# Performance work log

Hardware: AMD Instinct MI355X
Metric: run time of the kernel (lower is better)

Reference implementation:

```python
import jax, jax.numpy as jnp
import numpy as np

N_NODES = 40000
N_EDGES = 400000
N_GRAPHS = 64
CONV_DIM = 64
N_FEAT = 9
EDGE_DIM = 3
Z_DIM = 2 * CONV_DIM + EDGE_DIM  # 131


def setup_inputs() -> dict:
    key = jax.random.key(0)
    ks = jax.random.split(key, 32)
    def lin(k, fan_in, fan_out):
        b = 1.0 / np.sqrt(fan_in)
        kw, kb = jax.random.split(k)
        return (jax.random.uniform(kw, (fan_in, fan_out), jnp.float32, -b, b),
                jax.random.uniform(kb, (fan_out,), jnp.float32, -b, b))
    inp = {}
    inp['x'] = jax.random.normal(ks[0], (N_NODES, N_FEAT), jnp.float32)
    inp['edge_index_1'] = jax.random.randint(ks[1], (2, N_EDGES), 0, N_NODES, jnp.int32)
    inp['edge_index_2'] = jax.random.randint(ks[2], (2, N_EDGES), 0, N_NODES, jnp.int32)
    inp['weight_1'] = jax.random.normal(ks[3], (N_EDGES, EDGE_DIM), jnp.float32)
    inp['weight_2'] = jax.random.normal(ks[4], (N_EDGES, EDGE_DIM), jnp.float32)
    # sorted graph ids: 64 graphs of 625 nodes each
    inp['batch'] = jnp.repeat(jnp.arange(N_GRAPHS, dtype=jnp.int32), N_NODES // N_GRAPHS)
    # parameters (stored [in, out])
    inp['fc1_w'], inp['fc1_b'] = lin(ks[5], N_FEAT, CONV_DIM)
    inp['lin_f_w'], inp['lin_f_b'] = lin(ks[6], Z_DIM, CONV_DIM)
    inp['lin_s_w'], inp['lin_s_b'] = lin(ks[7], Z_DIM, CONV_DIM)
    inp['gru_w_ih'], inp['gru_b_ih'] = lin(ks[8], CONV_DIM, 3 * CONV_DIM)  # gate order r,z,n
    inp['gru_w_hh'], inp['gru_b_hh'] = lin(ks[9], CONV_DIM, 3 * CONV_DIM)
    inp['fcs_w'], inp['fcs_b'] = lin(ks[10], CONV_DIM, CONV_DIM)
    inp['fc2c_w'], inp['fc2c_b'] = lin(ks[11], CONV_DIM, 64)
    inp['fc3c_w'], inp['fc3c_b'] = lin(ks[12], 64, 2)
    inp['fc2d_w'], inp['fc2d_b'] = lin(ks[13], CONV_DIM, 64)
    inp['fc3d_w'], inp['fc3d_b'] = lin(ks[14], 64, 2)
    return inp


def _cgconv(x, edge_index, edge_attr, wf, bf, ws, bs):
    # CGConv, flow='target_to_source': x_i = x[row], x_j = x[col], aggregate (mean) at row
    row, col = edge_index[0], edge_index[1]
    z = jnp.concatenate([x[row], x[col], edge_attr], axis=-1)       # [E, 131]
    msg = jax.nn.sigmoid(z @ wf + bf) * jax.nn.softplus(z @ ws + bs)  # [E, C]
    agg = jax.ops.segment_sum(msg, row, num_segments=x.shape[0])
    cnt = jax.ops.segment_sum(jnp.ones((msg.shape[0],), msg.dtype), row, num_segments=x.shape[0])
    return x + agg / jnp.maximum(cnt, 1.0)[:, None]                  # residual


def _gru_step(xt, h, w_ih, w_hh, b_ih, b_hh):
    gi = xt @ w_ih + b_ih
    gh = h @ w_hh + b_hh
    ir, iz, inn = jnp.split(gi, 3, axis=-1)
    hr, hz, hn = jnp.split(gh, 3, axis=-1)
    r = jax.nn.sigmoid(ir + hr)
    zg = jax.nn.sigmoid(iz + hz)
    n = jnp.tanh(inn + r * hn)
    return (1.0 - zg) * n + zg * h


def reference(x, edge_index_1, edge_index_2, weight_1, weight_2, batch,
              fc1_w, fc1_b, lin_f_w, lin_f_b, lin_s_w, lin_s_b,
              gru_w_ih, gru_b_ih, gru_w_hh, gru_b_hh,
              fcs_w, fcs_b, fc2c_w, fc2c_b, fc3c_w, fc3c_b,
              fc2d_w, fc2d_b, fc3d_w, fc3d_b):
    x = jax.nn.relu(x @ fc1_w + fc1_b)          # dropout inactive (eval)
    h = x
    for _ in range(3):                          # 3 GRU refinement iterations
        m = jax.nn.relu(_cgconv(x, edge_index_2, weight_2, lin_f_w, lin_f_b, lin_s_w, lin_s_b))
        m = jax.nn.relu(_cgconv(m, edge_index_1, weight_1, lin_f_w, lin_f_b, lin_s_w, lin_s_b))
        h = _gru_step(m, h, gru_w_ih, gru_w_hh, gru_b_ih, gru_b_hh)
        x = h
    # first node index of each graph (batch is sorted)
    idx_ct = jnp.searchsorted(batch, jnp.arange(N_GRAPHS, dtype=batch.dtype))
    xg = x[idx_ct]                              # [B, C]
    xg = jax.nn.relu(xg @ fcs_w + fcs_b)
    xc = jax.nn.relu(xg @ fc2c_w + fc2c_b)
    x_class = jax.nn.sigmoid(xc @ fc3c_w + fc3c_b)
    xd = jax.nn.relu(xg @ fc2d_w + fc2d_b)
    x_delta = xd @ fc3d_w + fc3d_b
    return (x_class, x_delta)
```

## Files before the change

kernel.cpp:

```cpp
#include <hip/hip_runtime.h>
#include <hip/hip_bf16.h>
#include <hip/hip_fp16.h>
#include <math.h>

constexpr int NE = 400000;
constexpr int NN = 40000;
constexpr int CD = 64;
constexpr int NGRAPH = 64;
constexpr int SCAN_BLOCKS = (NN + 255) / 256;
constexpr int EBLK = (NE + 255) / 256;

typedef _Float16 f16x8 __attribute__((ext_vector_type(8)));
typedef float f32x4 __attribute__((ext_vector_type(4)));

__global__ void k_fc1(const float* __restrict__ x,
                      const float* __restrict__ w,
                      const float* __restrict__ b,
                      float* __restrict__ out) {
    int i = blockIdx.x * 256 + threadIdx.x;
    if (i >= NN * CD) return;
    int n = i >> 6, c = i & 63;
    float acc = b[c];
    #pragma unroll
    for (int k = 0; k < 9; ++k)
        acc = fmaf(x[n * 9 + k], w[k * 64 + c], acc);
    out[i] = fmaxf(acc, 0.f);
}

__global__ void k_count2(const int* __restrict__ ei1, const int* __restrict__ ei2,
                         int* __restrict__ cnt1, int* __restrict__ cnt2) {
    const int b = blockIdx.x;
    const bool s2 = (b >= EBLK);
    const int* ei = s2 ? ei2 : ei1;
    int* cnt = s2 ? cnt2 : cnt1;
    int e = (s2 ? b - EBLK : b) * 256 + threadIdx.x;
    if (e >= NE) return;
    atomicAdd(&cnt[ei[e]], 1);
}

__global__ void k_scan_part2(const int* __restrict__ cnt1, const int* __restrict__ cnt2,
                             int* __restrict__ part1, int* __restrict__ part2) {
    __shared__ int red[256];
    const int b = blockIdx.x;
    const bool s2 = (b >= SCAN_BLOCKS);
    const int* cnt = s2 ? cnt2 : cnt1;
    int* partials = s2 ? part2 : part1;
    const int bb = s2 ? b - SCAN_BLOCKS : b;
    const int tid = threadIdx.x;
    const int i = bb * 256 + tid;
    red[tid] = (i < NN) ? cnt[i] : 0;
    __syncthreads();
    for (int s = 128; s > 0; s >>= 1) {
        if (tid < s) red[tid] += red[tid + s];
        __syncthreads();
    }
    if (tid == 0) partials[bb] = red[0];
}

__global__ void k_scan_mid2(const int* __restrict__ part1, const int* __restrict__ part2,
                            int* __restrict__ offs1, int* __restrict__ offs2) {
    __shared__ int part[256];
    const bool s2 = (blockIdx.x == 1);
    const int* partials = s2 ? part2 : part1;
    int* offs = s2 ? offs2 : offs1;
    const int tid = threadIdx.x;
    const int v = (tid < SCAN_BLOCKS) ? partials[tid] : 0;
    part[tid] = v;
    __syncthreads();
    for (int off = 1; off < 256; off <<= 1) {
        int t = (tid >= off) ? part[tid - off] : 0;
        __syncthreads();
        part[tid] += t;
        __syncthreads();
    }
    if (tid < SCAN_BLOCKS) offs[tid] = part[tid] - v;
}

__global__ void k_scan_fill2(const int* __restrict__ cnt1, const int* __restrict__ cnt2,
                             const int* __restrict__ offs1, const int* __restrict__ offs2,
                             int* __restrict__ rs1, int* __restrict__ rs2,
                             int* __restrict__ cur1, int* __restrict__ cur2) {
    __shared__ int part[256];
    const int b = blockIdx.x;
    const bool s2 = (b >= SCAN_BLOCKS);
    const int* cnt = s2 ? cnt2 : cnt1;
    const int* offs = s2 ? offs2 : offs1;
    int* row_start = s2 ? rs2 : rs1;
    int* cursor = s2 ? cur2 : cur1;
    const int bb = s2 ? b - SCAN_BLOCKS : b;
    const int tid = threadIdx.x;
    const int i = bb * 256 + tid;
    const int v = (i < NN) ? cnt[i] : 0;
    part[tid] = v;
    __syncthreads();
    for (int off = 1; off < 256; off <<= 1) {
        int t = (tid >= off) ? part[tid - off] : 0;
        __syncthreads();
        part[tid] += t;
        __syncthreads();
    }
    const int excl = part[tid] - v + offs[bb];
    if (i < NN) { row_start[i] = excl; cursor[i] = excl; }
    if (i == NN - 1) row_start[NN] = NE;
}

__global__ void k_scatgath2(const int* __restrict__ ei1, const int* __restrict__ ei2,
                            const float* __restrict__ w1, const float* __restrict__ w2,
                            int* __restrict__ cur1, int* __restrict__ cur2,
                            uint4* __restrict__ rec1, uint4* __restrict__ rec2) {
    const int b = blockIdx.x;
    const bool s2 = (b >= EBLK);
    const int* ei = s2 ? ei2 : ei1;
    const float* ew = s2 ? w2 : w1;
    int* cursor = s2 ? cur2 : cur1;
    uint4* rec = s2 ? rec2 : rec1;
    int e = (s2 ? b - EBLK : b) * 256 + threadIdx.x;
    if (e >= NE) return;
    const int r = ei[e];
    const int c = ei[NE + e];
    const int pos = atomicAdd(&cursor[r], 1);
    const __half2 h01 = __floats2half2_rn(ew[3 * e], ew[3 * e + 1]);
    const __half2 h2  = __floats2half2_rn(ew[3 * e + 2], 0.f);
    rec[pos] = make_uint4((unsigned)(((r & 7) << 28) | c),
                          *(const unsigned*)&h01, *(const unsigned*)&h2, 0u);
}

__global__ void k_wt16(const float* __restrict__ lfw, const float* __restrict__ lsw,
                       _Float16* __restrict__ Wt) {
    const int k = blockIdx.x;
    const int c = threadIdx.x;
    float v;
    if (c < 64)       v = lfw[k * 64 + c];
    else if (c < 128) v = lsw[k * 64 + (c - 64)];
    else if (c < 192) v = lfw[(64 + k) * 64 + (c - 128)];
    else              v = lsw[(64 + k) * 64 + (c - 192)];
    Wt[c * 64 + k] = (_Float16)v;
}

__global__ void k_wtg16(const float* __restrict__ wih, const float* __restrict__ whh,
                        _Float16* __restrict__ WtG) {
    const int i = blockIdx.x * 256 + threadIdx.x;
    const int c = i >> 6, k = i & 63;
    const float v = (c < 192) ? wih[k * 192 + c] : whh[k * 192 + (c - 192)];
    WtG[c * 64 + k] = (_Float16)v;
}

__launch_bounds__(256, 4)
__global__ void k_proj_mfma(const float* __restrict__ x,
                            const _Float16* __restrict__ Wt,
                            const float* __restrict__ bfp, const float* __restrict__ bsp,
                            float* __restrict__ Pi, __half2* __restrict__ Pj16) {
    __shared__ _Float16 xs16[32][72];
    const int tid = threadIdx.x;
    const int n0 = blockIdx.x * 32;
    {
        const int n = tid >> 3, k0 = (tid & 7) * 8;
        const float4 a = *(const float4*)&x[(size_t)(n0 + n) * 64 + k0];
        const float4 b = *(const float4*)&x[(size_t)(n0 + n) * 64 + k0 + 4];
        f16x8 v;
        v[0] = (_Float16)a.x; v[1] = (_Float16)a.y; v[2] = (_Float16)a.z; v[3] = (_Float16)a.w;
        v[4] = (_Float16)b.x; v[5] = (_Float16)b.y; v[6] = (_Float16)b.z; v[7] = (_Float16)b.w;
        *(f16x8*)&xs16[n][k0] = v;
    }
    __syncthreads();
    const int l  = tid & 63;
    const int w  = tid >> 6;
    const int lr = l & 15;
    const int kb = l >> 4;
    const int nt = w & 1;
    const f16x8 A0 = *(const f16x8*)&xs16[nt * 16 + lr][kb * 8];
    const f16x8 A1 = *(const f16x8*)&xs16[nt * 16 + lr][32 + kb * 8];
    const int orow = n0 + nt * 16 + kb * 4;

    if (w < 2) {
        for (int ct = 0; ct < 8; ++ct) {
            const int col = ct * 16 + lr;
            const f16x8 B0 = *(const f16x8*)&Wt[col * 64 + kb * 8];
            const f16x8 B1 = *(const f16x8*)&Wt[col * 64 + 32 + kb * 8];
            f32x4 acc = {0.f, 0.f, 0.f, 0.f};
            acc = __builtin_amdgcn_mfma_f32_16x16x32_f16(A0, B0, acc, 0, 0, 0);
            acc = __builtin_amdgcn_mfma_f32_16x16x32_f16(A1, B1, acc, 0, 0, 0);
            const float bias = (col < 64) ? bfp[col] : bsp[col - 64];
            #pragma unroll
            for (int r = 0; r < 4; ++r)
                Pi[(size_t)(orow + r) * 128 + col] = acc[r] + bias;
        }
    } else {
        for (int pt = 0; pt < 4; ++pt) {
            const int colF = 128 + pt * 16 + lr;
            const int colS = 192 + pt * 16 + lr;
            const f16x8 BF0 = *(const f16x8*)&Wt[colF * 64 + kb * 8];
            const f16x8 BF1 = *(const f16x8*)&Wt[colF * 64 + 32 + kb * 8];
            const f16x8 BS0 = *(const f16x8*)&Wt[colS * 64 + kb * 8];
            const f16x8 BS1 = *(const f16x8*)&Wt[colS * 64 + 32 + kb * 8];
            f32x4 aF = {0.f, 0.f, 0.f, 0.f}, aS = {0.f, 0.f, 0.f, 0.f};
            aF = __builtin_amdgcn_mfma_f32_16x16x32_f16(A0, BF0, aF, 0, 0, 0);
            aF = __builtin_amdgcn_mfma_f32_16x16x32_f16(A1, BF1, aF, 0, 0, 0);
            aS = __builtin_amdgcn_mfma_f32_16x16x32_f16(A0, BS0, aS, 0, 0, 0);
            aS = __builtin_amdgcn_mfma_f32_16x16x32_f16(A1, BS1, aS, 0, 0, 0);
            const int cj = pt * 16 + lr;
            #pragma unroll
            for (int r = 0; r < 4; ++r)
                Pj16[(size_t)(orow + r) * 64 + cj] = __floats2half2_rn((float)aF[r], (float)aS[r]);
        }
    }
}

__launch_bounds__(256, 8)
__global__ void k_edge_range(const __half2* __restrict__ Pj,
                             const float* __restrict__ Pi,
                             const uint4* __restrict__ rec,
                             const float* __restrict__ wfe, const float* __restrict__ wse,
                             const int* __restrict__ rs,
                             const float* __restrict__ xin, float* __restrict__ out) {
    __shared__ __align__(8) __half2 piH[8][64];
    __shared__ __align__(16) float accS[8][8][64];
    __shared__ int rsS[9];
    const int tid = threadIdx.x;
    const int hw = tid >> 5;
    const int hb = hw & 1;
    const int wv = tid >> 6;
    const int c2 = (tid & 31) * 2;
    const int r0 = blockIdx.x * 8;
    for (int i = tid; i < 512; i += 256) {
        const int row = i >> 6, ch = i & 63;
        piH[row][ch] = __floats2half2_rn(Pi[(size_t)(r0 + row) * 128 + ch],
                                         Pi[(size_t)(r0 + row) * 128 + 64 + ch]);
    }
    for (int i = tid; i < 4096; i += 256)
        ((float*)accS)[i] = 0.f;
    if (tid < 9) rsS[tid] = rs[r0 + tid];
    __syncthreads();
    const float wf0a = wfe[c2],       wf0b = wfe[c2 + 1];
    const float wf1a = wfe[64 + c2],  wf1b = wfe[64 + c2 + 1];
    const float wf2a = wfe[128 + c2], wf2b = wfe[128 + c2 + 1];
    const float ws0a = wse[c2],       ws0b = wse[c2 + 1];
    const float ws1a = wse[64 + c2],  ws1b = wse[64 + c2 + 1];
    const float ws2a = wse[128 + c2], ws2b = wse[128 + c2 + 1];
    const int pbeg = rsS[0], pend = rsS[8];

#define EDGE_BODY(P)                                                              \
    {                                                                             \
        const uint4 rv = rec[P];                                                  \
        const float2 e01 = __half22float2(*(const __half2*)&rv.y);                \
        const float2 e2x = __half22float2(*(const __half2*)&rv.z);                \
        const int row = rv.x >> 28;                                               \
        const int joff = (int)((rv.x & 0x0FFFFFFFu) << 6) | c2;                   \
        const uint2 Jraw = *(const uint2*)(Pj + joff);                            \
        const float2 Ja = __half22float2(*(const __half2*)&Jraw.x);               \
        const float2 Jb = __half22float2(*(const __half2*)&Jraw.y);               \
        const uint2 PH = *(const uint2*)&piH[row][c2];                            \
        const float2 Pa = __half22float2(*(const __half2*)&PH.x);                 \
        const float2 Pb = __half22float2(*(const __half2*)&PH.y);                 \
        const float afa = Pa.x + Ja.x + e01.x * wf0a + e01.y * wf1a + e2x.x * wf2a; \
        const float asa = Pa.y + Ja.y + e01.x * ws0a + e01.y * ws1a + e2x.x * ws2a; \
        const float afb = Pb.x + Jb.x + e01.x * wf0b + e01.y * wf1b + e2x.x * wf2b; \
        const float asb = Pb.y + Jb.y + e01.x * ws0b + e01.y * ws1b + e2x.x * ws2b; \
        const float sga = __builtin_amdgcn_rcpf(1.f + __expf(-afa));              \
        const float spa = (asa > 20.f) ? asa : __logf(1.f + __expf(asa));         \
        const float sgb = __builtin_amdgcn_rcpf(1.f + __expf(-afb));              \
        const float spb = (asb > 20.f) ? asb : __logf(1.f + __expf(asb));         \
        float2 acc = *(const float2*)&accS[hw][row][c2];                          \
        acc.x = fmaf(sga, spa, acc.x);                                            \
        acc.y = fmaf(sgb, spb, acc.y);                                            \
        *(float2*)&accS[hw][row][c2] = acc;                                       \
    }

    int p0 = pbeg + 2 * wv;
    #pragma unroll 2
    for (; p0 + 2 <= pend; p0 += 8) {
        const int p = p0 + hb;
        EDGE_BODY(p)
    }
    {
        const int p = p0 + hb;
        if (p < pend) EDGE_BODY(p)
    }
#undef EDGE_BODY

    __syncthreads();
    for (int i = tid; i < 512; i += 256) {
        const int row = i >> 6, ch = i & 63;
        float s = 0.f;
        #pragma unroll
        for (int a = 0; a < 8; ++a) s += accS[a][row][ch];
        const int deg = rsS[row + 1] - rsS[row];
        const size_t o = (size_t)(r0 + row) * 64 + ch;
        out[o] = fmaxf(fmaf(s, 1.f / (float)max(deg, 1), xin[o]), 0.f);
    }
}

__global__ void k_gru_mfma(const float* __restrict__ m, float* __restrict__ h,
                           const _Float16* __restrict__ WtG,
                           const float* __restrict__ bih, const float* __restrict__ bhh) {
    __shared__ _Float16 ms16[32][72];
    __shared__ _Float16 hs16[32][72];
    __shared__ __align__(16) float hs32[32][64];
    const int tid = threadIdx.x;
    const int n0 = blockIdx.x * 32;
    {
        const int n = tid >> 3, k0 = (tid & 7) * 8;
        const float4 ma = *(const float4*)&m[(size_t)(n0 + n) * 64 + k0];
        const float4 mb = *(const float4*)&m[(size_t)(n0 + n) * 64 + k0 + 4];
        const float4 ha = *(const float4*)&h[(size_t)(n0 + n) * 64 + k0];
        const float4 hb = *(const float4*)&h[(size_t)(n0 + n) * 64 + k0 + 4];
        f16x8 mv, hv;
        mv[0] = (_Float16)ma.x; mv[1] = (_Float16)ma.y; mv[2] = (_Float16)ma.z; mv[3] = (_Float16)ma.w;
        mv[4] = (_Float16)mb.x; mv[5] = (_Float16)mb.y; mv[6] = (_Float16)mb.z; mv[7] = (_Float16)mb.w;
        hv[0] = (_Float16)ha.x; hv[1] = (_Float16)ha.y; hv[2] = (_Float16)ha.z; hv[3] = (_Float16)ha.w;
        hv[4] = (_Float16)hb.x; hv[5] = (_Float16)hb.y; hv[6] = (_Float16)hb.z; hv[7] = (_Float16)hb.w;
        *(f16x8*)&ms16[n][k0] = mv;
        *(f16x8*)&hs16[n][k0] = hv;
        *(float4*)&hs32[n][k0] = ha;
        *(float4*)&hs32[n][k0 + 4] = hb;
    }
    __syncthreads();
    const int l  = tid & 63;
    const int w  = tid >> 6;
    const int lr = l & 15;
    const int kb = l >> 4;
    const int nt = w & 1;
    const int cg = w >> 1;
    const f16x8 A0 = *(const f16x8*)&ms16[nt * 16 + lr][kb * 8];
    const f16x8 A1 = *(const f16x8*)&ms16[nt * 16 + lr][32 + kb * 8];
    const f16x8 H0 = *(const f16x8*)&hs16[nt * 16 + lr][kb * 8];
    const f16x8 H1 = *(const f16x8*)&hs16[nt * 16 + lr][32 + kb * 8];
    const int orow = n0 + nt * 16 + kb * 4;
    const int lrow = nt * 16 + kb * 4;

    #pragma unroll
    for (int t = 0; t < 2; ++t) {
        const int ct = cg + t * 2;
        const int c = ct * 16 + lr;
        const f16x8 BiR0 = *(const f16x8*)&WtG[(c)       * 64 + kb * 8];
        const f16x8 BiR1 = *(const f16x8*)&WtG[(c)       * 64 + 32 + kb * 8];
        const f16x8 BiZ0 = *(const f16x8*)&WtG[(64 + c)  * 64 + kb * 8];
        const f16x8 BiZ1 = *(const f16x8*)&WtG[(64 + c)  * 64 + 32 + kb * 8];
        const f16x8 BiN0 = *(const f16x8*)&WtG[(128 + c) * 64 + kb * 8];
        const f16x8 BiN1 = *(const f16x8*)&WtG[(128 + c) * 64 + 32 + kb * 8];
        const f16x8 BhR0 = *(const f16x8*)&WtG[(192 + c) * 64 + kb * 8];
        const f16x8 BhR1 = *(const f16x8*)&WtG[(192 + c) * 64 + 32 + kb * 8];
        const f16x8 BhZ0 = *(const f16x8*)&WtG[(256 + c) * 64 + kb * 8];
        const f16x8 BhZ1 = *(const f16x8*)&WtG[(256 + c) * 64 + 32 + kb * 8];
        const f16x8 BhN0 = *(const f16x8*)&WtG[(320 + c) * 64 + kb * 8];
        const f16x8 BhN1 = *(const f16x8*)&WtG[(320 + c) * 64 + 32 + kb * 8];
        f32x4 aIR = {0,0,0,0}, aIZ = {0,0,0,0}, aIN = {0,0,0,0};
        f32x4 aHR = {0,0,0,0}, aHZ = {0,0,0,0}, aHN = {0,0,0,0};
        aIR = __builtin_amdgcn_mfma_f32_16x16x32_f16(A0, BiR0, aIR, 0, 0, 0);
        aIR = __builtin_amdgcn_mfma_f32_16x16x32_f16(A1, BiR1, aIR, 0, 0, 0);
        aIZ = __builtin_amdgcn_mfma_f32_16x16x32_f16(A0, BiZ0, aIZ, 0, 0, 0);
        aIZ = __builtin_amdgcn_mfma_f32_16x16x32_f16(A1, BiZ1, aIZ, 0, 0, 0);
        aIN = __builtin_amdgcn_mfma_f32_16x16x32_f16(A0, BiN0, aIN, 0, 0, 0);
        aIN = __builtin_amdgcn_mfma_f32_16x16x32_f16(A1, BiN1, aIN, 0, 0, 0);
        aHR = __builtin_amdgcn_mfma_f32_16x16x32_f16(H0, BhR0, aHR, 0, 0, 0);
        aHR = __builtin_amdgcn_mfma_f32_16x16x32_f16(H1, BhR1, aHR, 0, 0, 0);
        aHZ = __builtin_amdgcn_mfma_f32_16x16x32_f16(H0, BhZ0, aHZ, 0, 0, 0);
        aHZ = __builtin_amdgcn_mfma_f32_16x16x32_f16(H1, BhZ1, aHZ, 0, 0, 0);
        aHN = __builtin_amdgcn_mfma_f32_16x16x32_f16(H0, BhN0, aHN, 0, 0, 0);
        aHN = __builtin_amdgcn_mfma_f32_16x16x32_f16(H1, BhN1, aHN, 0, 0, 0);
        const float bir = bih[c], biz = bih[64 + c], bin = bih[128 + c];
        const float bhr = bhh[c], bhz = bhh[64 + c], bhn = bhh[128 + c];
        #pragma unroll
        for (int r = 0; r < 4; ++r) {
            const float rg = 1.f / (1.f + __expf(-(((float)aIR[r] + bir) + ((float)aHR[r] + bhr))));
            const float zg = 1.f / (1.f + __expf(-(((float)aIZ[r] + biz) + ((float)aHZ[r] + bhz))));
            const float ng = tanhf(((float)aIN[r] + bin) + rg * ((float)aHN[r] + bhn));
            h[(size_t)(orow + r) * 64 + c] = (1.f - zg) * ng + zg * hs32[lrow + r][c];
        }
    }
}

__global__ void k_head(const float* __restrict__ h, const int* __restrict__ batch,
                       const float* __restrict__ fcsw, const float* __restrict__ fcsb,
                       const float* __restrict__ f2cw, const float* __restrict__ f2cb,
                       const float* __restrict__ f3cw, const float* __restrict__ f3cb,
                       const float* __restrict__ f2dw, const float* __restrict__ f2db,
                       const float* __restrict__ f3dw, const float* __restrict__ f3db,
                       float* __restrict__ out) {
    __shared__ float hsB[4096];
    __shared__ float waB[4096];
    __shared__ float wbB[4096];
    __shared__ float wcB[4096];
    __shared__ int sidx[64];
    const int tid = threadIdx.x;
    if (tid < 64) {
        int lo = 0, hi = NN;
        while (lo < hi) {
            int mid = (lo + hi) >> 1;
            if (batch[mid] < tid) lo = mid + 1; else hi = mid;
        }
        sidx[tid] = lo;
    }
    __syncthreads();
    for (int i = tid; i < 4096; i += 256) {
        int g = i >> 6, k = i & 63;
        hsB[i] = h[(size_t)sidx[g] * 64 + k];
        waB[i] = fcsw[i];
        wbB[i] = f2cw[i];
        wcB[i] = f2dw[i];
    }
    __syncthreads();
    float v[16];
    #pragma unroll
    for (int j = 0; j < 16; ++j) {
        const int i = j * 256 + tid, g = i >> 6, c = i & 63;
        float a = fcsb[c];
        for (int k = 0; k < 64; ++k) a = fmaf(hsB[g * 64 + k], waB[k * 64 + c], a);
        v[j] = fmaxf(a, 0.f);
    }
    __syncthreads();
    #pragma unroll
    for (int j = 0; j < 16; ++j) hsB[j * 256 + tid] = v[j];
    __syncthreads();
    float vc[16], vd[16];
    #pragma unroll
    for (int j = 0; j < 16; ++j) {
        const int i = j * 256 + tid, g = i >> 6, c = i & 63;
        float a1 = f2cb[c], a2 = f2db[c];
        for (int k = 0; k < 64; ++k) {
            const float xv = hsB[g * 64 + k];
            a1 = fmaf(xv, wbB[k * 64 + c], a1);
            a2 = fmaf(xv, wcB[k * 64 + c], a2);
        }
        vc[j] = fmaxf(a1, 0.f);
        vd[j] = fmaxf(a2, 0.f);
    }
    __syncthreads();
    #pragma unroll
    for (int j = 0; j < 16; ++j) {
        waB[j * 256 + tid] = vc[j];
        wbB[j * 256 + tid] = vd[j];
    }
    if (tid < 128) wcB[tid] = f3cw[tid];
    else           wcB[tid] = f3dw[tid - 128];
    __syncthreads();
    if (tid < 128) {
        int g = tid >> 1, j = tid & 1;
        float a = f3cb[j];
        for (int k = 0; k < 64; ++k) a = fmaf(waB[g * 64 + k], wcB[k * 2 + j], a);
        out[g * 2 + j] = 1.f / (1.f + expf(-a));
    } else {
        int t = tid - 128, g = t >> 1, j = t & 1;
        float a = f3db[j];
        for (int k = 0; k < 64; ++k) a = fmaf(wbB[g * 64 + k], wcB[128 + k * 2 + j], a);
        out[128 + g * 2 + j] = a;
    }
}

extern "C" void kernel_launch(void* const* d_in, const int* in_sizes, int n_in,
                              void* d_out, int out_size, void* d_ws, size_t ws_size,
                              hipStream_t stream) {
    (void)in_sizes; (void)n_in; (void)out_size; (void)ws_size;
    const float* x    = (const float*)d_in[0];
    const int* ei1    = (const int*)d_in[1];
    const int* ei2    = (const int*)d_in[2];
    const float* w1   = (const float*)d_in[3];
    const float* w2   = (const float*)d_in[4];
    const int* batch  = (const int*)d_in[5];
    const float* fc1w = (const float*)d_in[6];
    const float* fc1b = (const float*)d_in[7];
    const float* lfw  = (const float*)d_in[8];
    const float* lfb  = (const float*)d_in[9];
    const float* lsw  = (const float*)d_in[10];
    const float* lsb  = (const float*)d_in[11];
    const float* wih  = (const float*)d_in[12];
    const float* bih  = (const float*)d_in[13];
    const float* whh  = (const float*)d_in[14];
    const float* bhh  = (const float*)d_in[15];
    const float* fcsw = (const float*)d_in[16];
    const float* fcsb = (const float*)d_in[17];
    const float* f2cw = (const float*)d_in[18];
    const float* f2cb = (const float*)d_in[19];
    const float* f3cw = (const float*)d_in[20];
    const float* f3cb = (const float*)d_in[21];
    const float* f2dw = (const float*)d_in[22];
    const float* f2db = (const float*)d_in[23];
    const float* f3dw = (const float*)d_in[24];
    const float* f3db = (const float*)d_in[25];

    char* ws = (char*)d_ws;
    size_t off = 0;
    auto alloc = [&](size_t bytes) { char* p = ws + off; off += (bytes + 255) & ~size_t(255); return p; };
    float*   Pi    = (float*)alloc(size_t(NN) * 128 * 4);
    __half2* Pj16  = (__half2*)alloc(size_t(NN) * 64 * 4);
    float*   hbuf  = (float*)alloc(size_t(NN) * CD * 4);
    float*   mbuf  = (float*)alloc(size_t(NN) * CD * 4);
    _Float16* W16  = (_Float16*)alloc(256 * 64 * 2);
    _Float16* WG16 = (_Float16*)alloc(384 * 64 * 2);
    int*   cnt1  = (int*)alloc(size_t(NN) * 4);
    int*   cnt2  = (int*)alloc(size_t(NN) * 4);
    int*   rs1   = (int*)alloc(size_t(NN + 1) * 4);
    int*   rs2   = (int*)alloc(size_t(NN + 1) * 4);
    int*   cur1  = (int*)alloc(size_t(NN + 1) * 4);
    int*   cur2  = (int*)alloc(size_t(NN + 1) * 4);
    uint4* rec1  = (uint4*)alloc(size_t(NE) * 16);
    uint4* rec2  = (uint4*)alloc(size_t(NE) * 16);
    int*   part1 = (int*)alloc(256 * 4);
    int*   part2 = (int*)alloc(256 * 4);
    int*   offs1 = (int*)alloc(256 * 4);
    int*   offs2 = (int*)alloc(256 * 4);

    const int NB_NC = (NN * CD + 255) / 256;
    const int EDGE_BLOCKS = NN / 8;
    const int PROJ_BLOCKS = NN / 32;
    const int GRU_BLOCKS  = NN / 32;

    const float* lfe = lfw + 128 * 64;
    const float* lse = lsw + 128 * 64;

    hipMemsetAsync(cnt1, 0, size_t(NN) * 4 * 2 + 256, stream);
    k_count2<<<2 * EBLK, 256, 0, stream>>>(ei1, ei2, cnt1, cnt2);
    k_scan_part2<<<2 * SCAN_BLOCKS, 256, 0, stream>>>(cnt1, cnt2, part1, part2);
    k_scan_mid2<<<2, 256, 0, stream>>>(part1, part2, offs1, offs2);
    k_scan_fill2<<<2 * SCAN_BLOCKS, 256, 0, stream>>>(cnt1, cnt2, offs1, offs2, rs1, rs2, cur1, cur2);
    k_scatgath2<<<2 * EBLK, 256, 0, stream>>>(ei1, ei2, w1, w2, cur1, cur2, rec1, rec2);
    k_wt16<<<64, 256, 0, stream>>>(lfw, lsw, W16);
    k_wtg16<<<96, 256, 0, stream>>>(wih, whh, WG16);

    k_fc1<<<NB_NC, 256, 0, stream>>>(x, fc1w, fc1b, hbuf);

    for (int it = 0; it < 3; ++it) {
        k_proj_mfma<<<PROJ_BLOCKS, 256, 0, stream>>>(hbuf, W16, lfb, lsb, Pi, Pj16);
        k_edge_range<<<EDGE_BLOCKS, 256, 0, stream>>>(Pj16, Pi, rec2, lfe, lse, rs2, hbuf, mbuf);
        k_proj_mfma<<<PROJ_BLOCKS, 256, 0, stream>>>(mbuf, W16, lfb, lsb, Pi, Pj16);
        k_edge_range<<<EDGE_BLOCKS, 256, 0, stream>>>(Pj16, Pi, rec1, lfe, lse, rs1, mbuf, mbuf);
        k_gru_mfma<<<GRU_BLOCKS, 256, 0, stream>>>(mbuf, hbuf, WG16, bih, bhh);
    }

    k_head<<<1, 256, 0, stream>>>(hbuf, batch, fcsw, fcsb, f2cw, f2cb, f3cw, f3cb,
                                  f2dw, f2db, f3dw, f3db, (float*)d_out);
}
```

Measured before the change: 534.9 us.

## Replace per-row atomic scatter with two-level bucket sort for CSR edges

The edge scatter into CSR order now runs in two passes. The first pass scatters each edge into a 32-row bucket with a global atomic on a bucket cursor. The second pass sorts within each bucket using shared-memory atomics, replacing the per-row global atomics in the old scatter. This is meant to cut global atomic traffic and scattered 16-byte writes, at the cost of an extra temp buffer pass and two more kernel launches. It also raises the unroll factor of the edge aggregation loop from 2 to 4.

```diff
diff --git a/kernel.cpp b/kernel.cpp
--- a/kernel.cpp
+++ b/kernel.cpp
@@ -9,6 +9,7 @@
 constexpr int NGRAPH = 64;
 constexpr int SCAN_BLOCKS = (NN + 255) / 256;
 constexpr int EBLK = (NE + 255) / 256;
+constexpr int NBUCK = NN / 32;
 
 typedef _Float16 f16x8 __attribute__((ext_vector_type(8)));
 typedef float f32x4 __attribute__((ext_vector_type(4)));
@@ -78,15 +79,13 @@
 
 __global__ void k_scan_fill2(const int* __restrict__ cnt1, const int* __restrict__ cnt2,
                              const int* __restrict__ offs1, const int* __restrict__ offs2,
-                             int* __restrict__ rs1, int* __restrict__ rs2,
-                             int* __restrict__ cur1, int* __restrict__ cur2) {
+                             int* __restrict__ rs1, int* __restrict__ rs2) {
     __shared__ int part[256];
     const int b = blockIdx.x;
     const bool s2 = (b >= SCAN_BLOCKS);
     const int* cnt = s2 ? cnt2 : cnt1;
     const int* offs = s2 ? offs2 : offs1;
     int* row_start = s2 ? rs2 : rs1;
-    int* cursor = s2 ? cur2 : cur1;
     const int bb = s2 ? b - SCAN_BLOCKS : b;
     const int tid = threadIdx.x;
     const int i = bb * 256 + tid;
@@ -100,29 +99,60 @@
         __syncthreads();
     }
     const int excl = part[tid] - v + offs[bb];
-    if (i < NN) { row_start[i] = excl; cursor[i] = excl; }
+    if (i < NN) row_start[i] = excl;
     if (i == NN - 1) row_start[NN] = NE;
 }
 
-__global__ void k_scatgath2(const int* __restrict__ ei1, const int* __restrict__ ei2,
-                            const float* __restrict__ w1, const float* __restrict__ w2,
-                            int* __restrict__ cur1, int* __restrict__ cur2,
-                            uint4* __restrict__ rec1, uint4* __restrict__ rec2) {
+__global__ void k_bcur2(const int* __restrict__ rs1, const int* __restrict__ rs2,
+                        int* __restrict__ bcur1, int* __restrict__ bcur2) {
+    const int i = blockIdx.x * 256 + threadIdx.x;
+    if (i < NBUCK)      bcur1[i] = rs1[i * 32];
+    else if (i < 2 * NBUCK) bcur2[(i - NBUCK)] = rs2[(i - NBUCK) * 32];
+}
+
+__global__ void k_bucket2(const int* __restrict__ ei1, const int* __restrict__ ei2,
+                          const float* __restrict__ w1, const float* __restrict__ w2,
+                          int* __restrict__ bcur1, int* __restrict__ bcur2,
+                          uint4* __restrict__ tmp1, uint4* __restrict__ tmp2) {
     const int b = blockIdx.x;
     const bool s2 = (b >= EBLK);
     const int* ei = s2 ? ei2 : ei1;
     const float* ew = s2 ? w2 : w1;
-    int* cursor = s2 ? cur2 : cur1;
-    uint4* rec = s2 ? rec2 : rec1;
+    int* bcur = s2 ? bcur2 : bcur1;
+    uint4* tmp = s2 ? tmp2 : tmp1;
     int e = (s2 ? b - EBLK : b) * 256 + threadIdx.x;
     if (e >= NE) return;
     const int r = ei[e];
     const int c = ei[NE + e];
-    const int pos = atomicAdd(&cursor[r], 1);
+    const int pos = atomicAdd(&bcur[r >> 5], 1);
     const __half2 h01 = __floats2half2_rn(ew[3 * e], ew[3 * e + 1]);
     const __half2 h2  = __floats2half2_rn(ew[3 * e + 2], 0.f);
-    rec[pos] = make_uint4((unsigned)(((r & 7) << 28) | c),
+    tmp[pos] = make_uint4((unsigned)(((r & 31) << 26) | c),
                           *(const unsigned*)&h01, *(const unsigned*)&h2, 0u);
+}
+
+__global__ void k_bsort2(const uint4* __restrict__ tmp1, const uint4* __restrict__ tmp2,
+                         const int* __restrict__ rs1, const int* __restrict__ rs2,
+                         uint4* __restrict__ rec1, uint4* __restrict__ rec2) {
+    __shared__ int curs[32];
+    const int b = blockIdx.x;
+    const bool s2 = (b >= NBUCK);
+    const uint4* tmp = s2 ? tmp2 : tmp1;
+    const int* rs = s2 ? rs2 : rs1;
+    uint4* rec = s2 ? rec2 : rec1;
+    const int bb = s2 ? b - NBUCK : b;
+    const int R0 = bb * 32;
+    const int tid = threadIdx.x;
+    if (tid < 32) curs[tid] = rs[R0 + tid];
+    __syncthreads();
+    const int pbeg = rs[R0], pend = rs[R0 + 32];
+    for (int p = pbeg + tid; p < pend; p += 256) {
+        uint4 t = tmp[p];
+        const int lr = (int)(t.x >> 26);
+        const int pos = atomicAdd(&curs[lr], 1);
+        t.x = (unsigned)(((lr & 7) << 28) | (t.x & 0x03FFFFFFu));
+        rec[pos] = t;
+    }
 }
 
 __global__ void k_wt16(const float* __restrict__ lfw, const float* __restrict__ lsw,
@@ -267,7 +297,7 @@
     }
 
     int p0 = pbeg + 2 * wv;
-    #pragma unroll 2
+    #pragma unroll 4
     for (; p0 + 2 <= pend; p0 += 8) {
         const int p = p0 + hb;
         EDGE_BODY(p)
@@ -491,8 +521,10 @@
     int*   cnt2  = (int*)alloc(size_t(NN) * 4);
     int*   rs1   = (int*)alloc(size_t(NN + 1) * 4);
     int*   rs2   = (int*)alloc(size_t(NN + 1) * 4);
-    int*   cur1  = (int*)alloc(size_t(NN + 1) * 4);
-    int*   cur2  = (int*)alloc(size_t(NN + 1) * 4);
+    int*   bcur1 = (int*)alloc(size_t(NBUCK) * 4);
+    int*   bcur2 = (int*)alloc(size_t(NBUCK) * 4);
+    uint4* tmp1  = (uint4*)alloc(size_t(NE) * 16);
+    uint4* tmp2  = (uint4*)alloc(size_t(NE) * 16);
     uint4* rec1  = (uint4*)alloc(size_t(NE) * 16);
     uint4* rec2  = (uint4*)alloc(size_t(NE) * 16);
     int*   part1 = (int*)alloc(256 * 4);
@@ -512,8 +544,10 @@
     k_count2<<<2 * EBLK, 256, 0, stream>>>(ei1, ei2, cnt1, cnt2);
     k_scan_part2<<<2 * SCAN_BLOCKS, 256, 0, stream>>>(cnt1, cnt2, part1, part2);
     k_scan_mid2<<<2, 256, 0, stream>>>(part1, part2, offs1, offs2);
-    k_scan_fill2<<<2 * SCAN_BLOCKS, 256, 0, stream>>>(cnt1, cnt2, offs1, offs2, rs1, rs2, cur1, cur2);
-    k_scatgath2<<<2 * EBLK, 256, 0, stream>>>(ei1, ei2, w1, w2, cur1, cur2, rec1, rec2);
+    k_scan_fill2<<<2 * SCAN_BLOCKS, 256, 0, stream>>>(cnt1, cnt2, offs1, offs2, rs1, rs2);
+    k_bcur2<<<(2 * NBUCK + 255) / 256, 256, 0, stream>>>(rs1, rs2, bcur1, bcur2);
+    k_bucket2<<<2 * EBLK, 256, 0, stream>>>(ei1, ei2, w1, w2, bcur1, bcur2, tmp1, tmp2);
+    k_bsort2<<<2 * NBUCK, 256, 0, stream>>>(tmp1, tmp2, rs1, rs2, rec1, rec2);
     k_wt16<<<64, 256, 0, stream>>>(lfw, lsw, W16);
     k_wtg16<<<96, 256, 0, stream>>>(wih, whh, WG16);
 
```

Measured after the change: 626.2 us. +17.1%, slower.
